# Performance work log

Hardware: AMD Instinct MI355X
Metric: run time of the kernel (lower is better)

## Reference

```python
import jax, jax.numpy as jnp
import numpy as np

D, NH, DH, L, NCP, TW, NTP = 256, 8, 32, 4, 4, 2, 2
P = NCP + TW * NTP  # points per level per head
SHAPES = np.array([[4, 48, 64], [4, 24, 32], [4, 12, 16], [4, 6, 8]], dtype=np.int64)  # (T, H, W) per level


def _offset_biases():
    # Faithful to _reset_parameters: directional grid init for sampling-offset biases.
    thetas = np.arange(NH, dtype=np.float64) * (2.0 * np.pi / NH)
    grid = np.stack([np.cos(thetas), np.sin(thetas)], -1)
    grid = grid / np.abs(grid).max(-1, keepdims=True)
    curr = np.tile(grid.reshape(NH, 1, 1, 2), (1, L, NCP, 1))
    for i in range(NCP):
        curr[:, :, i, :] *= i + 1
    temp = np.tile(grid.reshape(NH, 1, 1, 1, 2), (1, L, TW, NTP, 1))
    init_offset = 0
    for pos, t in enumerate(range(1, TW + 1)):  # encoder default branch
        if t % 2:
            init_offset += 1
        for i in range(NTP):
            temp[:, :, pos, i, :] *= i + 1 + init_offset
    return curr.reshape(-1).astype(np.float32), temp.reshape(-1).astype(np.float32)


def setup_inputs() -> dict:
    key = jax.random.key(0)
    k = jax.random.split(key, 10)
    sizes = SHAPES[:, 0] * SHAPES[:, 1] * SHAPES[:, 2]
    Len_in = int(sizes.sum())  # 16320
    Lq, N = Len_in, 1
    b_so_np, b_tso_np = _offset_biases()
    return {
        "query": jax.random.normal(k[0], (N, Lq, D), jnp.float32),
        "reference_points": jax.random.uniform(k[1], (N, Lq, L, 2), jnp.float32),
        "temporal_offsets": jax.random.normal(k[2], (Lq, L, TW, 2), jnp.float32) * 0.02,
        "input_flatten": jax.random.normal(k[3], (N, Len_in, D), jnp.float32),
        "input_spatial_shapes": jnp.asarray(SHAPES),
        "input_level_start_index": jnp.asarray(np.concatenate([[0], np.cumsum(sizes)[:-1]]).astype(np.int64)),
        "W_so": jax.random.normal(k[4], (D, NH * L * NCP * 2), jnp.float32) * 0.01,
        "b_so": jnp.asarray(b_so_np),
        "W_tso": jax.random.normal(k[5], (D, NH * L * TW * NTP * 2), jnp.float32) * 0.01,
        "b_tso": jnp.asarray(b_tso_np),
        "W_aw": jax.random.normal(k[6], (D, NH * L * NCP), jnp.float32) * 0.02,
        "b_aw": jnp.zeros((NH * L * NCP,), jnp.float32),
        "W_taw": jax.random.normal(k[7], (D, NH * L * TW * NTP), jnp.float32) * 0.02,
        "b_taw": jnp.zeros((NH * L * TW * NTP,), jnp.float32),
        "W_v": jax.random.normal(k[8], (D, D), jnp.float32) / np.sqrt(D),
        "b_v": jnp.zeros((D,), jnp.float32),
        "W_o": jax.random.normal(k[9], (D, D), jnp.float32) / np.sqrt(D),
        "b_o": jnp.zeros((D,), jnp.float32),
    }


def _deform_core(value, loc, attn):
    # value: (N, Len_in, NH, DH); loc: (N, Lq, NH, L, P, 2) in [0,1]; attn: (N, Lq, NH, L, P)
    N, Lq = loc.shape[0], loc.shape[1]
    out = jnp.zeros((N, NH, Lq, DH), value.dtype)
    start = 0
    for l in range(L):  # small fixed level loop
        t, h, w = (int(s) for s in SHAPES[l])
        th = t * h  # frames stacked vertically -> grid is (T*H, W)
        npix = th * w
        v = value[:, start:start + npix].transpose(0, 2, 1, 3)  # (N, NH, npix, DH)
        # grid_sample semantics, align_corners=False, zero padding
        x = loc[:, :, :, l, :, 0] * w - 0.5
        y = loc[:, :, :, l, :, 1] * th - 0.5
        x0 = jnp.floor(x); y0 = jnp.floor(y)
        lx = x - x0; ly = y - y0
        x0i = x0.astype(jnp.int32); y0i = y0.astype(jnp.int32)

        def corner(xi, yi, wgt):
            inb = (xi >= 0) & (xi < w) & (yi >= 0) & (yi < th)
            idx = jnp.clip(yi, 0, th - 1) * w + jnp.clip(xi, 0, w - 1)  # (N,Lq,NH,P)
            idx = idx.transpose(0, 2, 1, 3).reshape(N, NH, Lq * P, 1)
            g = jnp.take_along_axis(v, idx, axis=2).reshape(N, NH, Lq, P, DH)
            wm = (wgt * inb).transpose(0, 2, 1, 3)  # (N,NH,Lq,P)
            return g * wm[..., None]

        samp = (corner(x0i, y0i, (1 - lx) * (1 - ly))
                + corner(x0i + 1, y0i, lx * (1 - ly))
                + corner(x0i, y0i + 1, (1 - lx) * ly)
                + corner(x0i + 1, y0i + 1, lx * ly))
        a = attn[:, :, :, l].transpose(0, 2, 1, 3)  # (N,NH,Lq,P)
        out = out + (samp * a[..., None]).sum(3)
        start += npix
    return out.transpose(0, 2, 1, 3).reshape(N, Lq, D)


def _forward(query, reference_points, temporal_offsets, input_flatten,
             W_so, b_so, W_tso, b_tso, W_aw, b_aw, W_taw, b_taw, W_v, b_v, W_o, b_o):
    N, Lq, _ = query.shape
    value = (input_flatten @ W_v + b_v).reshape(N, -1, NH, DH)
    cso = (query @ W_so + b_so).reshape(N, Lq, NH, L, NCP, 2)
    tso = (query @ W_tso + b_tso).reshape(N, Lq, NH, L, TW, NTP, 2)
    caw = (query @ W_aw + b_aw).reshape(N, Lq, NH, L * NCP)
    taw = (query @ W_taw + b_taw).reshape(N, Lq, NH, L * TW * NTP)
    aw = jax.nn.softmax(jnp.concatenate([caw, taw], -1), -1)  # joint softmax over curr+temporal
    attn = jnp.concatenate([aw[..., :L * NCP].reshape(N, Lq, NH, L, NCP),
                            aw[..., L * NCP:].reshape(N, Lq, NH, L, TW * NTP)], -1)
    # offset_normalizer = [W, T*H] per level
    norm = jnp.asarray(np.stack([SHAPES[:, 2], SHAPES[:, 0] * SHAPES[:, 1]], -1).astype(np.float32))
    tso_n = temporal_offsets[None, :, None, :, :, None, :] + tso / norm[None, None, None, :, None, None, :]
    tso_n = tso_n.reshape(N, Lq, NH, L, TW * NTP, 2)
    cso_n = cso / norm[None, None, None, :, None, :]
    loc = reference_points[:, :, None, :, None, :] + jnp.concatenate([cso_n, tso_n], 4)  # (N,Lq,NH,L,P,2)
    out = _deform_core(value, loc, attn)
    return out @ W_o + b_o


def reference(query, reference_points, temporal_offsets, input_flatten,
              input_spatial_shapes, input_level_start_index,
              W_so, b_so, W_tso, b_tso, W_aw, b_aw, W_taw, b_taw, W_v, b_v, W_o, b_o):
    return _forward(query, reference_points, temporal_offsets, input_flatten,
                    W_so, b_so, W_tso, b_tso, W_aw, b_aw, W_taw, b_taw, W_v, b_v, W_o, b_o)
```

## Files before the change

### kernel.cpp

```cpp
#include <hip/hip_runtime.h>


typedef unsigned short bfraw;
typedef __attribute__((ext_vector_type(4))) float f32x4;
typedef __attribute__((ext_vector_type(8))) short bf16x8;

__device__ __forceinline__ float bf2f(bfraw u) {
  union { unsigned int i; float f; } v; v.i = ((unsigned int)u) << 16; return v.f;
}
__device__ __forceinline__ bfraw f2bf(float f) {
  union { float f; unsigned int i; } v; v.f = f;
  unsigned int x = v.i;
  return (bfraw)((x + 0x7FFFu + ((x >> 16) & 1u)) >> 16);
}
__device__ __forceinline__ float lo16f(unsigned int w) {
  union { unsigned int i; float f; } v; v.i = w << 16; return v.f;
}
__device__ __forceinline__ float hi16f(unsigned int w) {
  union { unsigned int i; float f; } v; v.i = w & 0xFFFF0000u; return v.f;
}
__device__ __forceinline__ float loadx(const void* p, size_t i, int f32m) {
  if (f32m) return ((const float*)p)[i];
  else      return bf2f(((const bfraw*)p)[i]);
}
__device__ __forceinline__ unsigned pk2(float a, float b) {
  return (unsigned)f2bf(a) | ((unsigned)f2bf(b) << 16);
}

__global__ void detect_k(const void* q, int* flag) {
  const bfraw* b = (const bfraw*)q;
  const int t = threadIdx.x;
  int cnt = 0;
#pragma unroll
  for (int k = 0; k < 8; ++k) {
    float a = fabsf(bf2f(b[2 * (t * 8 + k)]));
    if (a > 0.0009765625f && a < 16.0f) ++cnt;
  }
#pragma unroll
  for (int m = 32; m >= 1; m >>= 1) cnt += __shfl_xor(cnt, m);
  if (t == 0) *flag = (cnt > 256) ? 0 : 1;
}

__global__ __launch_bounds__(256) void transpose_k(
    const void* W_v, const void* W_so, const void* W_tso,
    const void* W_aw, const void* W_taw, const void* W_o,
    const void* b_so, const void* b_tso, const void* b_aw, const void* b_taw,
    bfraw* __restrict__ WT, float* __restrict__ bcat, const int* flagp)
{
  const int f32m = *flagp;
  const int b = blockIdx.x, t = threadIdx.x;
  if (b < 1280) {
    float s;
    if (b < 256)       s = loadx(W_v, (size_t)t * 256 + b, f32m);
    else if (b < 1024) {
      const int rp = b - 256;
      if (rp < 256)      s = loadx(W_so,  (size_t)t * 256 + rp, f32m);
      else if (rp < 512) s = loadx(W_tso, (size_t)t * 256 + (rp - 256), f32m);
      else if (rp < 640) s = loadx(W_aw,  (size_t)t * 128 + (rp - 512), f32m);
      else               s = loadx(W_taw, (size_t)t * 128 + (rp - 640), f32m);
    } else               s = loadx(W_o,  (size_t)t * 256 + (b - 1024), f32m);
    WT[(size_t)b * 256 + t] = f2bf(s);
  } else {
    const int i = (b - 1280) * 256 + t;
    if (i < 768) {
      float s;
      if (i < 256)      s = loadx(b_so,  i, f32m);
      else if (i < 512) s = loadx(b_tso, i - 256, f32m);
      else if (i < 640) s = loadx(b_aw,  i - 512, f32m);
      else              s = loadx(b_taw, i - 640, f32m);
      bcat[i] = s;
    }
  }
}

__global__ __launch_bounds__(256) void gemm128_k(
    const void* __restrict__ A, const bfraw* __restrict__ WT,
    const void* __restrict__ bias, void* __restrict__ C,
    int M, int lda, int ldc, int r0a, int r0c,
    int amode, int cmode, int bmode, const int* __restrict__ flagp)
{
  __shared__ bfraw As[128][40];
  __shared__ bfraw Bs[128][40];
  const int f32m = *flagp;
  const int a_f32 = (amode == 0) ? f32m : 0;
  const int bm = blockIdx.x * 128;
  const int bn = blockIdx.y * 128;
  const int tid = threadIdx.x;
  const int wave = tid >> 6, lane = tid & 63;
  const int quad = lane >> 4, l16 = lane & 15;
  const int mb = (wave >> 1) * 64, nb = (wave & 1) * 64;
  const int srow = tid >> 1;
  const int sk = (tid & 1) * 16;

  int lr = bm + srow; if (lr >= M) lr = M - 1;
  const size_t aoff = (size_t)(r0a + lr) * lda;

  f32x4 acc[4][4] = {{{0.f}}};

  for (int k0 = 0; k0 < 256; k0 += 32) {
    uint4 pa0, pa1;
    if (a_f32) {
      const float* Af = (const float*)A + aoff + (k0 + sk);
      const float4 x0 = ((const float4*)Af)[0];
      const float4 x1 = ((const float4*)Af)[1];
      const float4 x2 = ((const float4*)Af)[2];
      const float4 x3 = ((const float4*)Af)[3];
      pa0.x = pk2(x0.x, x0.y); pa0.y = pk2(x0.z, x0.w);
      pa0.z = pk2(x1.x, x1.y); pa0.w = pk2(x1.z, x1.w);
      pa1.x = pk2(x2.x, x2.y); pa1.y = pk2(x2.z, x2.w);
      pa1.z = pk2(x3.x, x3.y); pa1.w = pk2(x3.z, x3.w);
    } else {
      const bfraw* Ab = (const bfraw*)A + aoff + (k0 + sk);
      pa0 = ((const uint4*)Ab)[0];
      pa1 = ((const uint4*)Ab)[1];
    }
    const bfraw* Bb = WT + (size_t)(bn + srow) * 256 + (k0 + sk);
    const uint4 pb0 = ((const uint4*)Bb)[0];
    const uint4 pb1 = ((const uint4*)Bb)[1];
    *(uint4*)&As[srow][sk]     = pa0;
    *(uint4*)&As[srow][sk + 8] = pa1;
    *(uint4*)&Bs[srow][sk]     = pb0;
    *(uint4*)&Bs[srow][sk + 8] = pb1;
    __syncthreads();

    bf16x8 af[4], bf[4];
#pragma unroll
    for (int i = 0; i < 4; ++i)
      af[i] = *(const bf16x8*)&As[mb + i * 16 + l16][quad * 8];
#pragma unroll
    for (int j = 0; j < 4; ++j)
      bf[j] = *(const bf16x8*)&Bs[nb + j * 16 + l16][quad * 8];
#pragma unroll
    for (int i = 0; i < 4; ++i)
#pragma unroll
      for (int j = 0; j < 4; ++j)
        acc[i][j] = __builtin_amdgcn_mfma_f32_16x16x32_bf16(af[i], bf[j], acc[i][j], 0, 0, 0);
    __syncthreads();
  }

#pragma unroll
  for (int j = 0; j < 4; ++j) {
    const int col = bn + nb + j * 16 + l16;
    const float bb = (bmode == 0) ? ((const float*)bias)[col] : loadx(bias, col, f32m);
#pragma unroll
    for (int i = 0; i < 4; ++i) {
#pragma unroll
      for (int r = 0; r < 4; ++r) {
        const int lrow = bm + mb + i * 16 + quad * 4 + r;
        if (lrow < M) {
          const float v = acc[i][j][r] + bb;
          const size_t off = (size_t)(r0c + lrow) * ldc + col;
          if (cmode == 0)  ((bfraw*)C)[off] = f2bf(v);
          else if (f32m)   ((float*)C)[off] = v;
          else             ((bfraw*)C)[off] = f2bf(v);
        }
      }
    }
  }
}

__global__ __launch_bounds__(256, 4) void sampler_k(
    bfraw* __restrict__ proj, const bfraw* __restrict__ value,
    const void* __restrict__ refp, const void* __restrict__ toff,
    int q0, const int* __restrict__ flagp)
{
  __shared__ int   s_idx[256][4];
  __shared__ float s_w[256][4];

  const int f32m = *flagp;
  const int q = q0 + blockIdx.x;
  const int tid = threadIdx.x;
  const int h = tid >> 5;
  const int sp = tid & 31;
  const int l = sp >> 3;
  const int p = sp & 7;

  const int W_i[4]  = {64, 32, 16, 8};
  const int TH_i[4] = {192, 96, 48, 24};
  const int ST_i[4] = {0, 12288, 15360, 16128};
  const float Wf  = (float)W_i[l];
  const float THf = (float)TH_i[l];

  bfraw* prow = proj + (size_t)(q - q0) * 768;

  const float logit = (p < 4) ? bf2f(prow[512 + h * 16 + l * 4 + p])
                              : bf2f(prow[640 + h * 16 + l * 4 + (p - 4)]);
  float mx = logit;
#pragma unroll
  for (int m = 16; m >= 1; m >>= 1) mx = fmaxf(mx, __shfl_xor(mx, m));
  const float e = __expf(logit - mx);
  float ssum = e;
#pragma unroll
  for (int m = 16; m >= 1; m >>= 1) ssum += __shfl_xor(ssum, m);
  const float attn = e / ssum;

  const float rx = loadx(refp, (size_t)(q * 4 + l) * 2 + 0, f32m);
  const float ry = loadx(refp, (size_t)(q * 4 + l) * 2 + 1, f32m);
  float ox, oy;
  if (p < 4) {
    ox = bf2f(prow[h * 32 + l * 8 + p * 2 + 0]) / Wf;
    oy = bf2f(prow[h * 32 + l * 8 + p * 2 + 1]) / THf;
  } else {
    const int pj = p - 4, tw = pj >> 1, j = pj & 1;
    ox = loadx(toff, (size_t)(q * 4 + l) * 4 + tw * 2 + 0, f32m) +
         bf2f(prow[256 + h * 32 + l * 8 + tw * 4 + j * 2 + 0]) / Wf;
    oy = loadx(toff, (size_t)(q * 4 + l) * 4 + tw * 2 + 1, f32m) +
         bf2f(prow[256 + h * 32 + l * 8 + tw * 4 + j * 2 + 1]) / THf;
  }
  const float x = (rx + ox) * Wf - 0.5f;
  const float y = (ry + oy) * THf - 0.5f;
  const float x0f = floorf(x), y0f = floorf(y);
  const float lx = x - x0f, ly = y - y0f;
  const int x0 = (int)x0f, y0 = (int)y0f;
  const int Wg = W_i[l], THg = TH_i[l], ST = ST_i[l];
  const float cwx[2] = {1.f - lx, lx};
  const float cwy[2] = {1.f - ly, ly};
#pragma unroll
  for (int c = 0; c < 4; ++c) {
    const int xi = x0 + (c & 1), yi = y0 + (c >> 1);
    const bool inb = (xi >= 0) & (xi < Wg) & (yi >= 0) & (yi < THg);
    const int xc = min(max(xi, 0), Wg - 1);
    const int yc = min(max(yi, 0), THg - 1);
    s_idx[tid][c] = ST + yc * Wg + xc;
    s_w[tid][c] = inb ? (attn * cwx[c & 1] * cwy[c >> 1]) : 0.f;
  }
  __syncthreads();

  {
    const int pg = sp >> 2;
    const int chq = sp & 3;
    const bfraw* vb = value + h * 32 + chq * 8;
    int   idx[16];
    float ww[16];
#pragma unroll
    for (int pt = 0; pt < 4; ++pt) {
      const int ds = h * 32 + pg * 4 + pt;
#pragma unroll
      for (int c = 0; c < 4; ++c) { idx[pt * 4 + c] = s_idx[ds][c]; ww[pt * 4 + c] = s_w[ds][c]; }
    }
    uint4 vv[16];
#pragma unroll
    for (int i = 0; i < 16; ++i) vv[i] = *(const uint4*)(vb + (size_t)idx[i] * 256);
    float acc[8] = {};
#pragma unroll
    for (int i = 0; i < 16; ++i) {
      const float w = ww[i]; const uint4 v = vv[i];
      acc[0] += w * lo16f(v.x); acc[1] += w * hi16f(v.x);
      acc[2] += w * lo16f(v.y); acc[3] += w * hi16f(v.y);
      acc[4] += w * lo16f(v.z); acc[5] += w * hi16f(v.z);
      acc[6] += w * lo16f(v.w); acc[7] += w * hi16f(v.w);
    }
#pragma unroll
    for (int m = 4; m <= 16; m <<= 1)
#pragma unroll
      for (int r = 0; r < 8; ++r)
        acc[r] += __shfl_xor(acc[r], m);
    if (pg == 0) {
      uint4 pk;
      pk.x = pk2(acc[0], acc[1]);
      pk.y = pk2(acc[2], acc[3]);
      pk.z = pk2(acc[4], acc[5]);
      pk.w = pk2(acc[6], acc[7]);
      *(uint4*)(prow + h * 32 + chq * 8) = pk;
    }
  }
}

extern "C" void kernel_launch(void* const* d_in, const int* in_sizes, int n_in,
                              void* d_out, int out_size, void* d_ws, size_t ws_size,
                              hipStream_t stream)
{
  const void* query  = d_in[0];
  const void* refp   = d_in[1];
  const void* toff   = d_in[2];
  const void* inflat = d_in[3];
  const void* W_so  = d_in[6];
  const void* b_so  = d_in[7];
  const void* W_tso = d_in[8];
  const void* b_tso = d_in[9];
  const void* W_aw  = d_in[10];
  const void* b_aw  = d_in[11];
  const void* W_taw = d_in[12];
  const void* b_taw = d_in[13];
  const void* W_v   = d_in[14];
  const void* b_v   = d_in[15];
  const void* W_o   = d_in[16];
  const void* b_o   = d_in[17];

  const int Lq = 16320;
  const size_t WT_B   = (size_t)1280 * 256 * 2;
  const size_t BCAT_B = 768 * 4;
  const size_t VAL_B  = (size_t)Lq * 256 * 2;
  bfraw* WT    = (bfraw*)d_ws;
  float* bcat  = (float*)((char*)d_ws + WT_B);
  bfraw* value = (bfraw*)((char*)d_ws + WT_B + BCAT_B);
  bfraw* proj  = (bfraw*)((char*)d_ws + WT_B + BCAT_B + VAL_B);
  int*   flag  = (int*)((char*)d_ws + ((ws_size - 4) & ~(size_t)3));

  const size_t fixed = WT_B + BCAT_B + VAL_B + 64;
  size_t avail = (ws_size > fixed) ? (ws_size - fixed) : 0;
  long long chk = (long long)(avail / (768 * 2));
  chk &= ~63LL;
  if (chk > Lq) chk = Lq;
  if (chk < 64) chk = 64;
  const int chunk = (int)chk;

  const bfraw* WvT    = WT;
  const bfraw* WprojT = WT + 256 * 256;
  const bfraw* WoT    = WT + 1024 * 256;

  const dim3 blk(256);
  detect_k<<<dim3(1), dim3(64), 0, stream>>>(query, flag);
  transpose_k<<<dim3(1283), blk, 0, stream>>>(W_v, W_so, W_tso, W_aw, W_taw, W_o,
                                              b_so, b_tso, b_aw, b_taw, WT, bcat, flag);
  gemm128_k<<<dim3((Lq + 127) / 128, 2), blk, 0, stream>>>(
      inflat, WvT, b_v, value, Lq, 256, 256, 0, 0, 0, 0, 1, flag);

  int q0 = 0;
  while (q0 < Lq) {
    int M = Lq - q0; if (M > chunk) M = chunk;
    gemm128_k<<<dim3((M + 127) / 128, 6), blk, 0, stream>>>(
        query, WprojT, bcat, proj, M, 256, 768, q0, 0, 0, 0, 0, flag);
    sampler_k<<<dim3(M), blk, 0, stream>>>(proj, value, refp, toff, q0, flag);
    gemm128_k<<<dim3((M + 127) / 128, 2), blk, 0, stream>>>(
        proj, WoT, b_o, d_out, M, 768, 256, 0, q0, 1, 1, 1, flag);
    q0 += M;
  }
}
```

Before: 254.6 us.

## Fuse value and projection GEMMs, drop chunking, inline dtype detection, retile sampler

Removes the separate dtype-detection kernel by having every kernel vote on the dtype from the first words of the query. The value and projection GEMMs are merged into one launch over a shared grid. The chunked loop is replaced by single full-size launches, which assumes the workspace holds the whole projection buffer. The sampler grid changes to 8 queries per block with heads on the y axis, and fewer launches and better-filled grids cut launch and tail overhead.

Result: faster. 247.6 us (-2.8%).

```diff
diff --git a/kernel.cpp b/kernel.cpp
--- a/kernel.cpp
+++ b/kernel.cpp
@@ -27,27 +27,24 @@
   return (unsigned)f2bf(a) | ((unsigned)f2bf(b) << 16);
 }
 
-__global__ void detect_k(const void* q, int* flag) {
-  const bfraw* b = (const bfraw*)q;
-  const int t = threadIdx.x;
+__device__ __forceinline__ int vote_f32(const void* q) {
+  const unsigned* p = (const unsigned*)q;
   int cnt = 0;
 #pragma unroll
-  for (int k = 0; k < 8; ++k) {
-    float a = fabsf(bf2f(b[2 * (t * 8 + k)]));
-    if (a > 0.0009765625f && a < 16.0f) ++cnt;
-  }
-#pragma unroll
-  for (int m = 32; m >= 1; m >>= 1) cnt += __shfl_xor(cnt, m);
-  if (t == 0) *flag = (cnt > 256) ? 0 : 1;
+  for (int i = 0; i < 16; ++i) {
+    const float a = fabsf(lo16f(p[i]));
+    cnt += (a > 0.0009765625f && a < 16.0f) ? 1 : 0;
+  }
+  return (cnt >= 8) ? 0 : 1;
 }
 
 __global__ __launch_bounds__(256) void transpose_k(
     const void* W_v, const void* W_so, const void* W_tso,
     const void* W_aw, const void* W_taw, const void* W_o,
     const void* b_so, const void* b_tso, const void* b_aw, const void* b_taw,
-    bfraw* __restrict__ WT, float* __restrict__ bcat, const int* flagp)
-{
-  const int f32m = *flagp;
+    bfraw* __restrict__ WT, float* __restrict__ bcat, const void* query)
+{
+  const int f32m = vote_f32(query);
   const int b = blockIdx.x, t = threadIdx.x;
   if (b < 1280) {
     float s;
@@ -73,18 +70,21 @@
   }
 }
 
-__global__ __launch_bounds__(256) void gemm128_k(
-    const void* __restrict__ A, const bfraw* __restrict__ WT,
-    const void* __restrict__ bias, void* __restrict__ C,
-    int M, int lda, int ldc, int r0a, int r0c,
-    int amode, int cmode, int bmode, const int* __restrict__ flagp)
+__global__ __launch_bounds__(256) void gemmVP_k(
+    const void* __restrict__ inflat, const void* __restrict__ query,
+    const bfraw* __restrict__ WT, const void* __restrict__ b_v,
+    const float* __restrict__ bcat,
+    bfraw* __restrict__ value, bfraw* __restrict__ proj, int M)
 {
   __shared__ bfraw As[128][40];
   __shared__ bfraw Bs[128][40];
-  const int f32m = *flagp;
-  const int a_f32 = (amode == 0) ? f32m : 0;
+  const int f32m = vote_f32(query);
+  const int y = blockIdx.y;
+  const void* A; bfraw* C; int ldc, wtb, colb, bmode;
+  if (y < 2) { A = inflat; C = value; ldc = 256; wtb = y * 128;           colb = y * 128;       bmode = 1; }
+  else       { A = query;  C = proj;  ldc = 768; wtb = 256 + (y - 2) * 128; colb = (y - 2) * 128; bmode = 0; }
+
   const int bm = blockIdx.x * 128;
-  const int bn = blockIdx.y * 128;
   const int tid = threadIdx.x;
   const int wave = tid >> 6, lane = tid & 63;
   const int quad = lane >> 4, l16 = lane & 15;
@@ -93,13 +93,13 @@
   const int sk = (tid & 1) * 16;
 
   int lr = bm + srow; if (lr >= M) lr = M - 1;
-  const size_t aoff = (size_t)(r0a + lr) * lda;
+  const size_t aoff = (size_t)lr * 256;
 
   f32x4 acc[4][4] = {{{0.f}}};
 
   for (int k0 = 0; k0 < 256; k0 += 32) {
     uint4 pa0, pa1;
-    if (a_f32) {
+    if (f32m) {
       const float* Af = (const float*)A + aoff + (k0 + sk);
       const float4 x0 = ((const float4*)Af)[0];
       const float4 x1 = ((const float4*)Af)[1];
@@ -114,7 +114,7 @@
       pa0 = ((const uint4*)Ab)[0];
       pa1 = ((const uint4*)Ab)[1];
     }
-    const bfraw* Bb = WT + (size_t)(bn + srow) * 256 + (k0 + sk);
+    const bfraw* Bb = WT + (size_t)(wtb + srow) * 256 + (k0 + sk);
     const uint4 pb0 = ((const uint4*)Bb)[0];
     const uint4 pb1 = ((const uint4*)Bb)[1];
     *(uint4*)&As[srow][sk]     = pa0;
@@ -140,8 +140,73 @@
 
 #pragma unroll
   for (int j = 0; j < 4; ++j) {
+    const int col = colb + nb + j * 16 + l16;
+    const float bb = bmode ? loadx(b_v, col, f32m) : bcat[col];
+#pragma unroll
+    for (int i = 0; i < 4; ++i) {
+#pragma unroll
+      for (int r = 0; r < 4; ++r) {
+        const int lrow = bm + mb + i * 16 + quad * 4 + r;
+        if (lrow < M) C[(size_t)lrow * ldc + col] = f2bf(acc[i][j][r] + bb);
+      }
+    }
+  }
+}
+
+__global__ __launch_bounds__(256) void gemmO_k(
+    const bfraw* __restrict__ proj, const bfraw* __restrict__ WT,
+    const void* __restrict__ b_o, void* __restrict__ Cout,
+    const void* __restrict__ query, int M)
+{
+  __shared__ bfraw As[128][40];
+  __shared__ bfraw Bs[128][40];
+  const int f32m = vote_f32(query);
+  const int bm = blockIdx.x * 128;
+  const int bn = blockIdx.y * 128;
+  const int tid = threadIdx.x;
+  const int wave = tid >> 6, lane = tid & 63;
+  const int quad = lane >> 4, l16 = lane & 15;
+  const int mb = (wave >> 1) * 64, nb = (wave & 1) * 64;
+  const int srow = tid >> 1;
+  const int sk = (tid & 1) * 16;
+
+  int lr = bm + srow; if (lr >= M) lr = M - 1;
+  const size_t aoff = (size_t)lr * 768;
+
+  f32x4 acc[4][4] = {{{0.f}}};
+
+  for (int k0 = 0; k0 < 256; k0 += 32) {
+    const bfraw* Ab = proj + aoff + (k0 + sk);
+    const uint4 pa0 = ((const uint4*)Ab)[0];
+    const uint4 pa1 = ((const uint4*)Ab)[1];
+    const bfraw* Bb = WT + (size_t)(1024 + bn + srow) * 256 + (k0 + sk);
+    const uint4 pb0 = ((const uint4*)Bb)[0];
+    const uint4 pb1 = ((const uint4*)Bb)[1];
+    *(uint4*)&As[srow][sk]     = pa0;
+    *(uint4*)&As[srow][sk + 8] = pa1;
+    *(uint4*)&Bs[srow][sk]     = pb0;
+    *(uint4*)&Bs[srow][sk + 8] = pb1;
+    __syncthreads();
+
+    bf16x8 af[4], bf[4];
+#pragma unroll
+    for (int i = 0; i < 4; ++i)
+      af[i] = *(const bf16x8*)&As[mb + i * 16 + l16][quad * 8];
+#pragma unroll
+    for (int j = 0; j < 4; ++j)
+      bf[j] = *(const bf16x8*)&Bs[nb + j * 16 + l16][quad * 8];
+#pragma unroll
+    for (int i = 0; i < 4; ++i)
+#pragma unroll
+      for (int j = 0; j < 4; ++j)
+        acc[i][j] = __builtin_amdgcn_mfma_f32_16x16x32_bf16(af[i], bf[j], acc[i][j], 0, 0, 0);
+    __syncthreads();
+  }
+
+#pragma unroll
+  for (int j = 0; j < 4; ++j) {
     const int col = bn + nb + j * 16 + l16;
-    const float bb = (bmode == 0) ? ((const float*)bias)[col] : loadx(bias, col, f32m);
+    const float bb = loadx(b_o, col, f32m);
 #pragma unroll
     for (int i = 0; i < 4; ++i) {
 #pragma unroll
@@ -149,10 +214,8 @@
         const int lrow = bm + mb + i * 16 + quad * 4 + r;
         if (lrow < M) {
           const float v = acc[i][j][r] + bb;
-          const size_t off = (size_t)(r0c + lrow) * ldc + col;
-          if (cmode == 0)  ((bfraw*)C)[off] = f2bf(v);
-          else if (f32m)   ((float*)C)[off] = v;
-          else             ((bfraw*)C)[off] = f2bf(v);
+          if (f32m) ((float*)Cout)[(size_t)lrow * 256 + col] = v;
+          else      ((bfraw*)Cout)[(size_t)lrow * 256 + col] = f2bf(v);
         }
       }
     }
@@ -162,18 +225,19 @@
 __global__ __launch_bounds__(256, 4) void sampler_k(
     bfraw* __restrict__ proj, const bfraw* __restrict__ value,
     const void* __restrict__ refp, const void* __restrict__ toff,
-    int q0, const int* __restrict__ flagp)
+    const void* __restrict__ query)
 {
   __shared__ int   s_idx[256][4];
   __shared__ float s_w[256][4];
 
-  const int f32m = *flagp;
-  const int q = q0 + blockIdx.x;
+  const int f32m = vote_f32(query);
+  const int h = blockIdx.y;
   const int tid = threadIdx.x;
-  const int h = tid >> 5;
+  const int qi = tid >> 5;
   const int sp = tid & 31;
   const int l = sp >> 3;
   const int p = sp & 7;
+  const int qg = blockIdx.x * 8 + qi;
 
   const int W_i[4]  = {64, 32, 16, 8};
   const int TH_i[4] = {192, 96, 48, 24};
@@ -181,7 +245,7 @@
   const float Wf  = (float)W_i[l];
   const float THf = (float)TH_i[l];
 
-  bfraw* prow = proj + (size_t)(q - q0) * 768;
+  bfraw* prow = proj + (size_t)qg * 768;
 
   const float logit = (p < 4) ? bf2f(prow[512 + h * 16 + l * 4 + p])
                               : bf2f(prow[640 + h * 16 + l * 4 + (p - 4)]);
@@ -194,17 +258,17 @@
   for (int m = 16; m >= 1; m >>= 1) ssum += __shfl_xor(ssum, m);
   const float attn = e / ssum;
 
-  const float rx = loadx(refp, (size_t)(q * 4 + l) * 2 + 0, f32m);
-  const float ry = loadx(refp, (size_t)(q * 4 + l) * 2 + 1, f32m);
+  const float rx = loadx(refp, (size_t)(qg * 4 + l) * 2 + 0, f32m);
+  const float ry = loadx(refp, (size_t)(qg * 4 + l) * 2 + 1, f32m);
   float ox, oy;
   if (p < 4) {
     ox = bf2f(prow[h * 32 + l * 8 + p * 2 + 0]) / Wf;
     oy = bf2f(prow[h * 32 + l * 8 + p * 2 + 1]) / THf;
   } else {
     const int pj = p - 4, tw = pj >> 1, j = pj & 1;
-    ox = loadx(toff, (size_t)(q * 4 + l) * 4 + tw * 2 + 0, f32m) +
+    ox = loadx(toff, (size_t)(qg * 4 + l) * 4 + tw * 2 + 0, f32m) +
          bf2f(prow[256 + h * 32 + l * 8 + tw * 4 + j * 2 + 0]) / Wf;
-    oy = loadx(toff, (size_t)(q * 4 + l) * 4 + tw * 2 + 1, f32m) +
+    oy = loadx(toff, (size_t)(qg * 4 + l) * 4 + tw * 2 + 1, f32m) +
          bf2f(prow[256 + h * 32 + l * 8 + tw * 4 + j * 2 + 1]) / THf;
   }
   const float x = (rx + ox) * Wf - 0.5f;
@@ -234,7 +298,7 @@
     float ww[16];
 #pragma unroll
     for (int pt = 0; pt < 4; ++pt) {
-      const int ds = h * 32 + pg * 4 + pt;
+      const int ds = qi * 32 + pg * 4 + pt;
 #pragma unroll
       for (int c = 0; c < 4; ++c) { idx[pt * 4 + c] = s_idx[ds][c]; ww[pt * 4 + c] = s_w[ds][c]; }
     }
@@ -295,35 +359,11 @@
   float* bcat  = (float*)((char*)d_ws + WT_B);
   bfraw* value = (bfraw*)((char*)d_ws + WT_B + BCAT_B);
   bfraw* proj  = (bfraw*)((char*)d_ws + WT_B + BCAT_B + VAL_B);
-  int*   flag  = (int*)((char*)d_ws + ((ws_size - 4) & ~(size_t)3));
-
-  const size_t fixed = WT_B + BCAT_B + VAL_B + 64;
-  size_t avail = (ws_size > fixed) ? (ws_size - fixed) : 0;
-  long long chk = (long long)(avail / (768 * 2));
-  chk &= ~63LL;
-  if (chk > Lq) chk = Lq;
-  if (chk < 64) chk = 64;
-  const int chunk = (int)chk;
-
-  const bfraw* WvT    = WT;
-  const bfraw* WprojT = WT + 256 * 256;
-  const bfraw* WoT    = WT + 1024 * 256;
 
   const dim3 blk(256);
-  detect_k<<<dim3(1), dim3(64), 0, stream>>>(query, flag);
   transpose_k<<<dim3(1283), blk, 0, stream>>>(W_v, W_so, W_tso, W_aw, W_taw, W_o,
-                                              b_so, b_tso, b_aw, b_taw, WT, bcat, flag);
-  gemm128_k<<<dim3((Lq + 127) / 128, 2), blk, 0, stream>>>(
-      inflat, WvT, b_v, value, Lq, 256, 256, 0, 0, 0, 0, 1, flag);
-
-  int q0 = 0;
-  while (q0 < Lq) {
-    int M = Lq - q0; if (M > chunk) M = chunk;
-    gemm128_k<<<dim3((M + 127) / 128, 6), blk, 0, stream>>>(
-        query, WprojT, bcat, proj, M, 256, 768, q0, 0, 0, 0, 0, flag);
-    sampler_k<<<dim3(M), blk, 0, stream>>>(proj, value, refp, toff, q0, flag);
-    gemm128_k<<<dim3((M + 127) / 128, 2), blk, 0, stream>>>(
-        proj, WoT, b_o, d_out, M, 768, 256, 0, q0, 1, 1, 1, flag);
-    q0 += M;
-  }
-}
+                                              b_so, b_tso, b_aw, b_taw, WT, bcat, query);
+  gemmVP_k<<<dim3(128, 8), blk, 0, stream>>>(inflat, query, WT, b_v, bcat, value, proj, Lq);
+  sampler_k<<<dim3(Lq / 8, 8), blk, 0, stream>>>(proj, value, refp, toff, query);
+  gemmO_k<<<dim3(128, 2), blk, 0, stream>>>(proj, WT, b_o, d_out, query, Lq);
+}
```
